# Optimization experiments

Measured on AMD Instinct MI355X. Metric: run time of the kernel, lower is better.

The kernel has to match this reference:

```python
import jax, jax.numpy as jnp
import numpy as np


def setup_inputs() -> dict:
    key = jax.random.key(0)
    ks = jax.random.split(key, 8)
    B, IN, H, OUT = 8192, 1024, 2048, 1024
    SIGMA_MIN, SIGMA_MAX, PHASE = 0.9, 0.999, 2.0 * np.pi
    # recurrence decay params, initialized as in the torch module
    rng = np.random.RandomState(0)
    u1 = rng.random_sample(H)
    u2 = rng.random_sample(H)
    v = -0.5 * np.log(u1 * (SIGMA_MAX ** 2 - SIGMA_MIN ** 2) + SIGMA_MIN ** 2)
    theta = u2 * PHASE
    scale_b = 1.0 / np.sqrt(IN)
    scale_c = 1.0 / np.sqrt(H)
    return {
        "x": jax.random.normal(ks[0], (B, IN), dtype=jnp.float32),
        "h_prev": jax.random.normal(ks[1], (B, H), dtype=jnp.float32),
        "Br": jax.random.normal(ks[2], (H, IN), dtype=jnp.float32) * scale_b,
        "Bi": jax.random.normal(ks[3], (H, IN), dtype=jnp.float32) * scale_b,
        "Cr": jax.random.normal(ks[4], (OUT, H), dtype=jnp.float32) * scale_c,
        "Ci": jax.random.normal(ks[5], (OUT, H), dtype=jnp.float32) * scale_c,
        "v_log": jnp.asarray(np.log(v), dtype=jnp.float32),
        "theta_log": jnp.asarray(np.log(theta), dtype=jnp.float32),
    }


def reference(x, h_prev, Br, Bi, Cr, Ci, v_log, theta_log):
    # effective diagonal recurrence weight w = exp(-exp(v_log) + i*exp(theta_log))
    mag = jnp.exp(-jnp.exp(v_log))            # [H]
    ang = jnp.exp(theta_log)                  # [H]
    wr = mag * jnp.cos(ang)
    wi = mag * jnp.sin(ang)
    # h = B(x) + h_prev * w  (h_prev is real -> imag part comes only from wi)
    # complexLinear on real x: real = x@Br^T, imag = x@Bi^T
    hr = jnp.einsum('bi,hi->bh', x, Br) + h_prev * wr   # [B,H]
    hi = jnp.einsum('bi,hi->bh', x, Bi) + h_prev * wi   # [B,H]
    # out = Re(C(h)) = hr@Cr^T - hi@Ci^T
    out = jnp.einsum('bh,oh->bo', hr, Cr) - jnp.einsum('bh,oh->bo', hi, Ci)
    return out
```

## Files before the change

kernel.cpp:

```cpp
#include <hip/hip_runtime.h>
#include <stdint.h>

typedef unsigned short u16;
typedef short bf16x8 __attribute__((ext_vector_type(8)));
typedef float f32x4 __attribute__((ext_vector_type(4)));

typedef void as1_void __attribute__((address_space(1)));
typedef void as3_void __attribute__((address_space(3)));

__device__ inline u16 f32_to_bf16(float f) {
    uint32_t u = __builtin_bit_cast(uint32_t, f);
    u += 0x7fffu + ((u >> 16) & 1u);
    return (u16)(u >> 16);
}

__device__ inline void gld_lds16(const void* g, void* l) {
    __builtin_amdgcn_global_load_lds((as1_void*)g, (as3_void*)l, 16, 0, 0);
}



__global__ void prep_kernel(const float* __restrict__ Cr, const float* __restrict__ Ci,
                            const float* __restrict__ Br, const float* __restrict__ Bi,
                            const float* __restrict__ v_log, const float* __restrict__ th_log,
                            u16* __restrict__ Ccat, u16* __restrict__ Bcat,
                            u16* __restrict__ Cwbf)
{
    __shared__ float t[32][33];
    const int b = blockIdx.x, tid = threadIdx.x;

    if (b < 4096) {
        int i = b * 256 + tid;
        int e = i * 4;
        int o = e >> 12;
        int k = e & 4095;
        float4 f; float s;
        if (k < 2048) { f = *(const float4*)(Cr + (size_t)o * 2048 + k);          s =  1.f; }
        else          { f = *(const float4*)(Ci + (size_t)o * 2048 + (k - 2048)); s = -1.f; }
        ushort4 u;
        u.x = f32_to_bf16(s * f.x); u.y = f32_to_bf16(s * f.y);
        u.z = f32_to_bf16(s * f.z); u.w = f32_to_bf16(s * f.w);
        ((ushort4*)Ccat)[i] = u;
    } else if (b < 8192) {
        int b2 = b - 4096;
        const float* src = (b2 & 2048) ? Bi : Br;
        int colOff = (b2 & 2048) ? 2048 : 0;
        int c0 = (b2 & 31) * 32, r0 = ((b2 >> 5) & 63) * 32;
        int tx = tid & 31, ty = tid >> 5;
#pragma unroll
        for (int j = 0; j < 4; j++)
            t[ty + j * 8][tx] = src[(size_t)(r0 + ty + j * 8) * 1024 + c0 + tx];
        __syncthreads();
#pragma unroll
        for (int j = 0; j < 4; j++)
            Bcat[(size_t)(c0 + ty + j * 8) * 4096 + colOff + r0 + tx] =
                f32_to_bf16(t[tx][ty + j * 8]);
    } else {
        int j = (b - 8192) * 256 + tid;
        int e = j * 4;
        int o = e >> 11;
        int h = e & 2047;
        float4 cr = *(const float4*)(Cr + (size_t)o * 2048 + h);
        float4 ci = *(const float4*)(Ci + (size_t)o * 2048 + h);
        float4 vl = *(const float4*)(v_log + h);
        float4 tl = *(const float4*)(th_log + h);
        float mag, ang, wr, wi;
        ushort4 u;
        mag = expf(-expf(vl.x)); ang = expf(tl.x); wr = mag * cosf(ang); wi = mag * sinf(ang);
        u.x = f32_to_bf16(cr.x * wr - ci.x * wi);
        mag = expf(-expf(vl.y)); ang = expf(tl.y); wr = mag * cosf(ang); wi = mag * sinf(ang);
        u.y = f32_to_bf16(cr.y * wr - ci.y * wi);
        mag = expf(-expf(vl.z)); ang = expf(tl.z); wr = mag * cosf(ang); wi = mag * sinf(ang);
        u.z = f32_to_bf16(cr.z * wr - ci.z * wi);
        mag = expf(-expf(vl.w)); ang = expf(tl.w); wr = mag * cosf(ang); wi = mag * sinf(ang);
        u.w = f32_to_bf16(cr.w * wr - ci.w * wi);
        ((ushort4*)Cwbf)[j] = u;
    }
}


__global__ void reduce_cast_kernel(const float* __restrict__ partials,
                                   const float* __restrict__ x,
                                   const float* __restrict__ h_prev,
                                   u16* __restrict__ Wmain,
                                   u16* __restrict__ x_bf,
                                   u16* __restrict__ hp_bf)
{
    const int b = blockIdx.x, tid = threadIdx.x;
    if (b < 1024) {
        int i = b * 256 + tid;
        int e = i * 4;
        float4 s = *(const float4*)(partials + e);
#pragma unroll
        for (int z = 1; z < 8; z++) {
            float4 p = *(const float4*)(partials + ((size_t)z << 20) + e);
            s.x += p.x; s.y += p.y; s.z += p.z; s.w += p.w;
        }
        ushort4 u;
        u.x = f32_to_bf16(s.x); u.y = f32_to_bf16(s.y);
        u.z = f32_to_bf16(s.z); u.w = f32_to_bf16(s.w);
        ((ushort4*)Wmain)[i] = u;
    } else if (b < 9216) {
        int i = (b - 1024) * 256 + tid;
        float4 f = ((const float4*)x)[i];
        ushort4 o;
        o.x = f32_to_bf16(f.x); o.y = f32_to_bf16(f.y);
        o.z = f32_to_bf16(f.z); o.w = f32_to_bf16(f.w);
        ((ushort4*)x_bf)[i] = o;
    } else {
        int i = (b - 9216) * 256 + tid;
        float4 f = ((const float4*)h_prev)[i];
        ushort4 o;
        o.x = f32_to_bf16(f.x); o.y = f32_to_bf16(f.y);
        o.z = f32_to_bf16(f.z); o.w = f32_to_bf16(f.w);
        ((ushort4*)hp_bf)[i] = o;
    }
}


__global__ void reduce_only_kernel(const float* __restrict__ partials,
                                   u16* __restrict__ Wmain) {
    int i = blockIdx.x * blockDim.x + threadIdx.x;
    int e = i * 4;
    float4 s = *(const float4*)(partials + e);
#pragma unroll
    for (int z = 1; z < 8; z++) {
        float4 p = *(const float4*)(partials + ((size_t)z << 20) + e);
        s.x += p.x; s.y += p.y; s.z += p.z; s.w += p.w;
    }
    ushort4 u;
    u.x = f32_to_bf16(s.x); u.y = f32_to_bf16(s.y);
    u.z = f32_to_bf16(s.z); u.w = f32_to_bf16(s.w);
    ((ushort4*)Wmain)[i] = u;
}

__global__ void cast_both_kernel(const float* __restrict__ x,
                                 const float* __restrict__ h_prev,
                                 u16* __restrict__ dst) {
    const int n4x = 8192 * 1024 / 4;
    int i = blockIdx.x * blockDim.x + threadIdx.x;
    float4 f = (i < n4x) ? ((const float4*)x)[i] : ((const float4*)h_prev)[i - n4x];
    ushort4 o;
    o.x = f32_to_bf16(f.x); o.y = f32_to_bf16(f.y);
    o.z = f32_to_bf16(f.z); o.w = f32_to_bf16(f.w);
    ((ushort4*)dst)[i] = o;
}


__global__ __launch_bounds__(256)
void gemm_splitk_kernel(const u16* __restrict__ A, const u16* __restrict__ B,
                        float* __restrict__ partials)
{
    __shared__ __align__(16) u16 ldsA[128 * 64];
    __shared__ __align__(16) u16 ldsB[128 * 64];
    const int K = 4096;

    const int tid = threadIdx.x, wid = tid >> 6, lane = tid & 63;
    const int quad = lane >> 4, l16 = lane & 15;
    const int wm = wid >> 1, wn = wid & 1;
    const int bm = blockIdx.y, bn = blockIdx.x, bz = blockIdx.z;
    const int kb = bz * 512;

    const u16* gA[4]; const u16* gB[4];
    u16 *lA[4], *lB[4];
#pragma unroll
    for (int t = 0; t < 4; t++) {
        int s = wid * 256 + t * 64 + lane;
        int sr = s >> 3;
        int sj = (s & 7) ^ (sr & 7);
        lA[t] = ldsA + s * 8;
        lB[t] = ldsB + s * 8;
        gA[t] = A + (size_t)(bm * 128 + sr) * K + sj * 8 + kb;
        gB[t] = B + (size_t)(bn * 128 + sr) * K + sj * 8 + kb;
    }

    const f32x4 fz = {0.f, 0.f, 0.f, 0.f};
    f32x4 acc[4][4];
#pragma unroll
    for (int i = 0; i < 4; i++)
#pragma unroll
        for (int j = 0; j < 4; j++) acc[i][j] = fz;

    for (int k0 = 0; k0 < 512; k0 += 64) {
        __syncthreads();
#pragma unroll
        for (int t = 0; t < 4; t++) {
            gld_lds16(gA[t] + k0, lA[t]);
            gld_lds16(gB[t] + k0, lB[t]);
        }
        __syncthreads();
#pragma unroll
        for (int ks = 0; ks < 2; ks++) {
            bf16x8 af[4], bfr[4];
#pragma unroll
            for (int i = 0; i < 4; i++) {
                int r = wm * 64 + i * 16 + l16;
                af[i] = *(const bf16x8*)(ldsA + (r * 8 + ((ks * 4 + quad) ^ (r & 7))) * 8);
            }
#pragma unroll
            for (int j = 0; j < 4; j++) {
                int r = wn * 64 + j * 16 + l16;
                bfr[j] = *(const bf16x8*)(ldsB + (r * 8 + ((ks * 4 + quad) ^ (r & 7))) * 8);
            }
#pragma unroll
            for (int i = 0; i < 4; i++)
#pragma unroll
                for (int j = 0; j < 4; j++)
                    acc[i][j] = __builtin_amdgcn_mfma_f32_16x16x32_bf16(af[i], bfr[j], acc[i][j], 0, 0, 0);
        }
    }

    float* P = partials + ((size_t)bz << 20);
    const int gm = bm * 128 + wm * 64, gn = bn * 128 + wn * 64;
#pragma unroll
    for (int i = 0; i < 4; i++)
#pragma unroll
        for (int j = 0; j < 4; j++) {
            int col = gn + j * 16 + l16;
#pragma unroll
            for (int r = 0; r < 4; r++)
                P[(size_t)(gm + i * 16 + quad * 4 + r) * 1024 + col] = acc[i][j][r];
        }
}


__global__ __launch_bounds__(512)
void gemm_main_kernel(const u16* __restrict__ Axb, const u16* __restrict__ Ahb,
                      const u16* __restrict__ Bw,  const u16* __restrict__ Bcw,
                      float* __restrict__ out)
{
    __shared__ __align__(16) u16 lds[3][24576];

    const int tid = threadIdx.x, wid = tid >> 6, lane = tid & 63;
    const int quad = lane >> 4, l16 = lane & 15;
    const int wm = wid >> 1, wn = wid & 1;
    const int id = blockIdx.x;
    const int bm = id & 31, bn = id >> 5;

    int srA[4], sjA[4], srB[2], sjB[2];
#pragma unroll
    for (int q = 0; q < 4; q++) {
        int s = q * 512 + tid;
        srA[q] = s >> 3;
        sjA[q] = (s & 7) ^ (srA[q] & 7);
    }
#pragma unroll
    for (int q = 0; q < 2; q++) {
        int s = q * 512 + tid;
        srB[q] = s >> 3;
        sjB[q] = (s & 7) ^ (srB[q] & 7);
    }

    u16* buf0 = &lds[0][0];
    u16* buf1 = &lds[1][0];
    u16* buf2 = &lds[2][0];

    const f32x4 fz = {0.f, 0.f, 0.f, 0.f};
    f32x4 acc[4][4];
#pragma unroll
    for (int i = 0; i < 4; i++)
#pragma unroll
        for (int j = 0; j < 4; j++) acc[i][j] = fz;

    auto stage = [&](int tt, u16* buf) {
        const u16* Ab; const u16* Bb; int KS, koff;
        if (tt < 16) { Ab = Axb; Bb = Bw;  KS = 1024; koff = tt * 64; }
        else         { Ab = Ahb; Bb = Bcw; KS = 2048; koff = (tt - 16) * 64; }
#pragma unroll
        for (int q = 0; q < 4; q++)
            gld_lds16(Ab + (size_t)(bm * 256 + srA[q]) * KS + koff + sjA[q] * 8,
                      buf + (q * 512 + tid) * 8);
#pragma unroll
        for (int q = 0; q < 2; q++)
            gld_lds16(Bb + (size_t)(bn * 128 + srB[q]) * KS + koff + sjB[q] * 8,
                      buf + 16384 + (q * 512 + tid) * 8);
    };

    auto compute = [&](const u16* buf) {
#pragma unroll
        for (int ks = 0; ks < 2; ks++) {
            bf16x8 af[4], bfr[4];
#pragma unroll
            for (int i = 0; i < 4; i++) {
                int r = wm * 64 + i * 16 + l16;
                af[i] = *(const bf16x8*)(buf + (r * 8 + ((ks * 4 + quad) ^ (r & 7))) * 8);
            }
#pragma unroll
            for (int j = 0; j < 4; j++) {
                int r = wn * 64 + j * 16 + l16;
                bfr[j] = *(const bf16x8*)(buf + 16384 + (r * 8 + ((ks * 4 + quad) ^ (r & 7))) * 8);
            }
            __builtin_amdgcn_s_setprio(1);
#pragma unroll
            for (int i = 0; i < 4; i++)
#pragma unroll
                for (int j = 0; j < 4; j++)
                    acc[i][j] = __builtin_amdgcn_mfma_f32_16x16x32_bf16(af[i], bfr[j], acc[i][j], 0, 0, 0);
            __builtin_amdgcn_s_setprio(0);
        }
    };

#define PUBLISH(N)                                          \
    asm volatile("s_waitcnt vmcnt(" #N ")" ::: "memory");   \
    __builtin_amdgcn_s_barrier();                           \
    asm volatile("" ::: "memory")

    stage(0, buf0);
    stage(1, buf1);
    PUBLISH(6);

#pragma unroll 1
    for (int it = 0; it < 15; it++) {
        stage(3 * it + 2, buf2); compute(buf0); PUBLISH(6);
        stage(3 * it + 3, buf0); compute(buf1); PUBLISH(6);
        stage(3 * it + 4, buf1); compute(buf2); PUBLISH(6);
    }
    stage(47, buf2); compute(buf0); PUBLISH(6);
    compute(buf1); PUBLISH(0);
    compute(buf2);
#undef PUBLISH

    const int gm = bm * 256 + wm * 64, gn = bn * 128 + wn * 64;
#pragma unroll
    for (int i = 0; i < 4; i++)
#pragma unroll
        for (int j = 0; j < 4; j++) {
            int col = gn + j * 16 + l16;
#pragma unroll
            for (int r = 0; r < 4; r++)
                out[(size_t)(gm + i * 16 + quad * 4 + r) * 1024 + col] = acc[i][j][r];
        }
}


extern "C" void kernel_launch(void* const* d_in, const int* in_sizes, int n_in,
                              void* d_out, int out_size, void* d_ws, size_t ws_size,
                              hipStream_t stream)
{
    const float* x      = (const float*)d_in[0];
    const float* h_prev = (const float*)d_in[1];
    const float* Br     = (const float*)d_in[2];
    const float* Bi     = (const float*)d_in[3];
    const float* Cr     = (const float*)d_in[4];
    const float* Ci     = (const float*)d_in[5];
    const float* v_log  = (const float*)d_in[6];
    const float* th_log = (const float*)d_in[7];
    float* out = (float*)d_out;

    const size_t MB = 1024 * 1024;
    if (ws_size < 54 * MB) return;
    const bool big = (ws_size >= 86 * MB);

    char* ws = (char*)d_ws;
    u16*   Ccat     = (u16*)ws;
    u16*   Bcat     = (u16*)(ws + 8 * MB);
    float* partials = (float*)(ws + 16 * MB);
    u16*   x_bf     = (u16*)ws;
    u16*   Wmain    = (u16*)(ws + 48 * MB);
    u16*   Cwbf     = (u16*)(ws + 50 * MB);
    u16*   hp_bf    = big ? (u16*)(ws + 54 * MB) : (u16*)(ws + 16 * MB);

    prep_kernel<<<10240, 256, 0, stream>>>(Cr, Ci, Br, Bi, v_log, th_log,
                                           Ccat, Bcat, Cwbf);
    gemm_splitk_kernel<<<dim3(8, 8, 8), 256, 0, stream>>>(Ccat, Bcat, partials);
    if (big) {
        reduce_cast_kernel<<<25600, 256, 0, stream>>>(partials, x, h_prev,
                                                      Wmain, x_bf, hp_bf);
    } else {
        reduce_only_kernel<<<1024, 256, 0, stream>>>(partials, Wmain);
        cast_both_kernel<<<24576, 256, 0, stream>>>(x, h_prev, x_bf);
    }
    gemm_main_kernel<<<256, 512, 0, stream>>>(x_bf, hp_bf, Wmain, Cwbf, out);
}
```

Baseline: 246.2 us.

## Fuse fp32-to-bf16 activation cast into main GEMM A-tile loading

Removes the separate cast kernel for x and h_prev. The main GEMM now loads the fp32 activations into registers, converts them to bf16 and writes them into LDS itself, while B tiles still use direct global-to-LDS loads. This avoids writing and rereading roughly 48 MB of bf16 intermediates and drops a kernel launch. In exchange the GEMM reads twice the bytes for A, adds VALU conversion work and register pressure, and replaces the vmcnt-based pipelining with full __syncthreads, which may expose load latency.

```diff
diff --git a/kernel.cpp b/kernel.cpp
--- a/kernel.cpp
+++ b/kernel.cpp
@@ -79,45 +79,6 @@
 }
 
 
-__global__ void reduce_cast_kernel(const float* __restrict__ partials,
-                                   const float* __restrict__ x,
-                                   const float* __restrict__ h_prev,
-                                   u16* __restrict__ Wmain,
-                                   u16* __restrict__ x_bf,
-                                   u16* __restrict__ hp_bf)
-{
-    const int b = blockIdx.x, tid = threadIdx.x;
-    if (b < 1024) {
-        int i = b * 256 + tid;
-        int e = i * 4;
-        float4 s = *(const float4*)(partials + e);
-#pragma unroll
-        for (int z = 1; z < 8; z++) {
-            float4 p = *(const float4*)(partials + ((size_t)z << 20) + e);
-            s.x += p.x; s.y += p.y; s.z += p.z; s.w += p.w;
-        }
-        ushort4 u;
-        u.x = f32_to_bf16(s.x); u.y = f32_to_bf16(s.y);
-        u.z = f32_to_bf16(s.z); u.w = f32_to_bf16(s.w);
-        ((ushort4*)Wmain)[i] = u;
-    } else if (b < 9216) {
-        int i = (b - 1024) * 256 + tid;
-        float4 f = ((const float4*)x)[i];
-        ushort4 o;
-        o.x = f32_to_bf16(f.x); o.y = f32_to_bf16(f.y);
-        o.z = f32_to_bf16(f.z); o.w = f32_to_bf16(f.w);
-        ((ushort4*)x_bf)[i] = o;
-    } else {
-        int i = (b - 9216) * 256 + tid;
-        float4 f = ((const float4*)h_prev)[i];
-        ushort4 o;
-        o.x = f32_to_bf16(f.x); o.y = f32_to_bf16(f.y);
-        o.z = f32_to_bf16(f.z); o.w = f32_to_bf16(f.w);
-        ((ushort4*)hp_bf)[i] = o;
-    }
-}
-
-
 __global__ void reduce_only_kernel(const float* __restrict__ partials,
                                    u16* __restrict__ Wmain) {
     int i = blockIdx.x * blockDim.x + threadIdx.x;
@@ -132,18 +93,6 @@
     u.x = f32_to_bf16(s.x); u.y = f32_to_bf16(s.y);
     u.z = f32_to_bf16(s.z); u.w = f32_to_bf16(s.w);
     ((ushort4*)Wmain)[i] = u;
-}
-
-__global__ void cast_both_kernel(const float* __restrict__ x,
-                                 const float* __restrict__ h_prev,
-                                 u16* __restrict__ dst) {
-    const int n4x = 8192 * 1024 / 4;
-    int i = blockIdx.x * blockDim.x + threadIdx.x;
-    float4 f = (i < n4x) ? ((const float4*)x)[i] : ((const float4*)h_prev)[i - n4x];
-    ushort4 o;
-    o.x = f32_to_bf16(f.x); o.y = f32_to_bf16(f.y);
-    o.z = f32_to_bf16(f.z); o.w = f32_to_bf16(f.w);
-    ((ushort4*)dst)[i] = o;
 }
 
 
@@ -225,7 +174,7 @@
 
 
 __global__ __launch_bounds__(512)
-void gemm_main_kernel(const u16* __restrict__ Axb, const u16* __restrict__ Ahb,
+void gemm_main_kernel(const float* __restrict__ Xf, const float* __restrict__ Hf,
                       const u16* __restrict__ Bw,  const u16* __restrict__ Bcw,
                       float* __restrict__ out)
 {
@@ -262,18 +211,43 @@
 #pragma unroll
         for (int j = 0; j < 4; j++) acc[i][j] = fz;
 
-    auto stage = [&](int tt, u16* buf) {
-        const u16* Ab; const u16* Bb; int KS, koff;
-        if (tt < 16) { Ab = Axb; Bb = Bw;  KS = 1024; koff = tt * 64; }
-        else         { Ab = Ahb; Bb = Bcw; KS = 2048; koff = (tt - 16) * 64; }
-#pragma unroll
-        for (int q = 0; q < 4; q++)
-            gld_lds16(Ab + (size_t)(bm * 256 + srA[q]) * KS + koff + sjA[q] * 8,
-                      buf + (q * 512 + tid) * 8);
+    auto stageB = [&](int tt, u16* buf) {
+        const u16* Bb; int KS, koff;
+        if (tt < 16) { Bb = Bw;  KS = 1024; koff = tt * 64; }
+        else         { Bb = Bcw; KS = 2048; koff = (tt - 16) * 64; }
 #pragma unroll
         for (int q = 0; q < 2; q++)
             gld_lds16(Bb + (size_t)(bn * 128 + srB[q]) * KS + koff + sjB[q] * 8,
                       buf + 16384 + (q * 512 + tid) * 8);
+    };
+
+    float4 areg[4][2];
+    auto loadA = [&](int tt) {
+        const float* Af; int KS, koff;
+        if (tt < 16) { Af = Xf; KS = 1024; koff = tt * 64; }
+        else         { Af = Hf; KS = 2048; koff = (tt - 16) * 64; }
+#pragma unroll
+        for (int q = 0; q < 4; q++) {
+            const float* p = Af + (size_t)(bm * 256 + srA[q]) * KS + koff + sjA[q] * 8;
+            areg[q][0] = *(const float4*)(p);
+            areg[q][1] = *(const float4*)(p + 4);
+        }
+    };
+
+    auto writeA = [&](u16* buf) {
+#pragma unroll
+        for (int q = 0; q < 4; q++) {
+            bf16x8 v;
+            v[0] = (short)f32_to_bf16(areg[q][0].x);
+            v[1] = (short)f32_to_bf16(areg[q][0].y);
+            v[2] = (short)f32_to_bf16(areg[q][0].z);
+            v[3] = (short)f32_to_bf16(areg[q][0].w);
+            v[4] = (short)f32_to_bf16(areg[q][1].x);
+            v[5] = (short)f32_to_bf16(areg[q][1].y);
+            v[6] = (short)f32_to_bf16(areg[q][1].z);
+            v[7] = (short)f32_to_bf16(areg[q][1].w);
+            *(bf16x8*)(buf + ((size_t)q * 512 + tid) * 8) = v;
+        }
     };
 
     auto compute = [&](const u16* buf) {
@@ -300,25 +274,19 @@
         }
     };
 
-#define PUBLISH(N)                                          \
-    asm volatile("s_waitcnt vmcnt(" #N ")" ::: "memory");   \
-    __builtin_amdgcn_s_barrier();                           \
-    asm volatile("" ::: "memory")
-
-    stage(0, buf0);
-    stage(1, buf1);
-    PUBLISH(6);
+    stageB(0, buf0); loadA(0); writeA(buf0);
+    stageB(1, buf1); loadA(1); writeA(buf1);
+    __syncthreads();
 
 #pragma unroll 1
     for (int it = 0; it < 15; it++) {
-        stage(3 * it + 2, buf2); compute(buf0); PUBLISH(6);
-        stage(3 * it + 3, buf0); compute(buf1); PUBLISH(6);
-        stage(3 * it + 4, buf1); compute(buf2); PUBLISH(6);
-    }
-    stage(47, buf2); compute(buf0); PUBLISH(6);
-    compute(buf1); PUBLISH(0);
+        stageB(3 * it + 2, buf2); loadA(3 * it + 2); compute(buf0); writeA(buf2); __syncthreads();
+        stageB(3 * it + 3, buf0); loadA(3 * it + 3); compute(buf1); writeA(buf0); __syncthreads();
+        stageB(3 * it + 4, buf1); loadA(3 * it + 4); compute(buf2); writeA(buf1); __syncthreads();
+    }
+    stageB(47, buf2); loadA(47); compute(buf0); writeA(buf2); __syncthreads();
+    compute(buf1);
     compute(buf2);
-#undef PUBLISH
 
     const int gm = bm * 256 + wm * 64, gn = bn * 128 + wn * 64;
 #pragma unroll
@@ -349,26 +317,17 @@
 
     const size_t MB = 1024 * 1024;
     if (ws_size < 54 * MB) return;
-    const bool big = (ws_size >= 86 * MB);
 
     char* ws = (char*)d_ws;
     u16*   Ccat     = (u16*)ws;
     u16*   Bcat     = (u16*)(ws + 8 * MB);
     float* partials = (float*)(ws + 16 * MB);
-    u16*   x_bf     = (u16*)ws;
     u16*   Wmain    = (u16*)(ws + 48 * MB);
     u16*   Cwbf     = (u16*)(ws + 50 * MB);
-    u16*   hp_bf    = big ? (u16*)(ws + 54 * MB) : (u16*)(ws + 16 * MB);
 
     prep_kernel<<<10240, 256, 0, stream>>>(Cr, Ci, Br, Bi, v_log, th_log,
                                            Ccat, Bcat, Cwbf);
     gemm_splitk_kernel<<<dim3(8, 8, 8), 256, 0, stream>>>(Ccat, Bcat, partials);
-    if (big) {
-        reduce_cast_kernel<<<25600, 256, 0, stream>>>(partials, x, h_prev,
-                                                      Wmain, x_bf, hp_bf);
-    } else {
-        reduce_only_kernel<<<1024, 256, 0, stream>>>(partials, Wmain);
-        cast_both_kernel<<<24576, 256, 0, stream>>>(x, h_prev, x_bf);
-    }
-    gemm_main_kernel<<<256, 512, 0, stream>>>(x_bf, hp_bf, Wmain, Cwbf, out);
-}
+    reduce_only_kernel<<<1024, 256, 0, stream>>>(partials, Wmain);
+    gemm_main_kernel<<<256, 512, 0, stream>>>(x, h_prev, Wmain, Cwbf, out);
+}
```

Result: slower. 291.0 us (+18.2%).

## Fuse split-K weight GEMM with activation bf16 cast in one launch

Applied to the files above, without the earlier changes.

Adds a combined kernel where the first 512 blocks compute the split-K weight-product GEMM and the remaining blocks cast x and h_prev to bf16 with a grid-stride loop. The memory-bound cast is meant to overlap with the compute-bound GEMM instead of running in a separate serialized phase, and the reduce kernel becomes reduce-only. It needs a larger workspace (102 MB) to keep separate buffers for x_bf and hp_bf, and otherwise falls back to the old path. Cast blocks may contend for bandwidth and compute units with the GEMM blocks.

```diff
diff --git a/kernel.cpp b/kernel.cpp
--- a/kernel.cpp
+++ b/kernel.cpp
@@ -79,6 +79,120 @@
 }
 
 
+__device__ __forceinline__
+void splitk_block(const u16* __restrict__ A, const u16* __restrict__ B,
+                  float* __restrict__ partials,
+                  int bm, int bn, int bz, int tid,
+                  u16* ldsA, u16* ldsB)
+{
+    const int K = 4096;
+    const int wid = tid >> 6, lane = tid & 63;
+    const int quad = lane >> 4, l16 = lane & 15;
+    const int wm = wid >> 1, wn = wid & 1;
+    const int kb = bz * 512;
+
+    const u16* gA[4]; const u16* gB[4];
+    u16 *lA[4], *lB[4];
+#pragma unroll
+    for (int t = 0; t < 4; t++) {
+        int s = wid * 256 + t * 64 + lane;
+        int sr = s >> 3;
+        int sj = (s & 7) ^ (sr & 7);
+        lA[t] = ldsA + s * 8;
+        lB[t] = ldsB + s * 8;
+        gA[t] = A + (size_t)(bm * 128 + sr) * K + sj * 8 + kb;
+        gB[t] = B + (size_t)(bn * 128 + sr) * K + sj * 8 + kb;
+    }
+
+    const f32x4 fz = {0.f, 0.f, 0.f, 0.f};
+    f32x4 acc[4][4];
+#pragma unroll
+    for (int i = 0; i < 4; i++)
+#pragma unroll
+        for (int j = 0; j < 4; j++) acc[i][j] = fz;
+
+    for (int k0 = 0; k0 < 512; k0 += 64) {
+        __syncthreads();
+#pragma unroll
+        for (int t = 0; t < 4; t++) {
+            gld_lds16(gA[t] + k0, lA[t]);
+            gld_lds16(gB[t] + k0, lB[t]);
+        }
+        __syncthreads();
+#pragma unroll
+        for (int ks = 0; ks < 2; ks++) {
+            bf16x8 af[4], bfr[4];
+#pragma unroll
+            for (int i = 0; i < 4; i++) {
+                int r = wm * 64 + i * 16 + l16;
+                af[i] = *(const bf16x8*)(ldsA + (r * 8 + ((ks * 4 + quad) ^ (r & 7))) * 8);
+            }
+#pragma unroll
+            for (int j = 0; j < 4; j++) {
+                int r = wn * 64 + j * 16 + l16;
+                bfr[j] = *(const bf16x8*)(ldsB + (r * 8 + ((ks * 4 + quad) ^ (r & 7))) * 8);
+            }
+#pragma unroll
+            for (int i = 0; i < 4; i++)
+#pragma unroll
+                for (int j = 0; j < 4; j++)
+                    acc[i][j] = __builtin_amdgcn_mfma_f32_16x16x32_bf16(af[i], bfr[j], acc[i][j], 0, 0, 0);
+        }
+    }
+
+    float* P = partials + ((size_t)bz << 20);
+    const int gm = bm * 128 + wm * 64, gn = bn * 128 + wn * 64;
+#pragma unroll
+    for (int i = 0; i < 4; i++)
+#pragma unroll
+        for (int j = 0; j < 4; j++) {
+            int col = gn + j * 16 + l16;
+#pragma unroll
+            for (int r = 0; r < 4; r++)
+                P[(size_t)(gm + i * 16 + quad * 4 + r) * 1024 + col] = acc[i][j][r];
+        }
+}
+
+__global__ __launch_bounds__(256)
+void gemm_splitk_kernel(const u16* __restrict__ A, const u16* __restrict__ B,
+                        float* __restrict__ partials)
+{
+    __shared__ __align__(16) u16 ldsA[128 * 64];
+    __shared__ __align__(16) u16 ldsB[128 * 64];
+    splitk_block(A, B, partials, blockIdx.y, blockIdx.x, blockIdx.z, threadIdx.x,
+                 ldsA, ldsB);
+}
+
+__global__ __launch_bounds__(256)
+void splitk_cast_kernel(const u16* __restrict__ A, const u16* __restrict__ B,
+                        float* __restrict__ partials,
+                        const float* __restrict__ x, const float* __restrict__ h_prev,
+                        u16* __restrict__ x_bf, u16* __restrict__ hp_bf)
+{
+    __shared__ __align__(16) u16 ldsA[128 * 64];
+    __shared__ __align__(16) u16 ldsB[128 * 64];
+    const int id = blockIdx.x, tid = threadIdx.x;
+    if (id < 512) {
+        splitk_block(A, B, partials, (id >> 3) & 7, id & 7, id >> 6, tid,
+                     ldsA, ldsB);
+        return;
+    }
+    const int cid = id - 512;
+    const int n4x = 8192 * 1024 / 4;
+    const int n4  = n4x + 8192 * 2048 / 4;
+#pragma unroll 1
+    for (int j = cid * 256 + tid; j < n4; j += 2048 * 256) {
+        float4 f; ushort4 o;
+        if (j < n4x) { f = ((const float4*)x)[j]; }
+        else         { f = ((const float4*)h_prev)[j - n4x]; }
+        o.x = f32_to_bf16(f.x); o.y = f32_to_bf16(f.y);
+        o.z = f32_to_bf16(f.z); o.w = f32_to_bf16(f.w);
+        if (j < n4x) ((ushort4*)x_bf)[j] = o;
+        else         ((ushort4*)hp_bf)[j - n4x] = o;
+    }
+}
+
+
 __global__ void reduce_cast_kernel(const float* __restrict__ partials,
                                    const float* __restrict__ x,
                                    const float* __restrict__ h_prev,
@@ -117,7 +231,6 @@
     }
 }
 
-
 __global__ void reduce_only_kernel(const float* __restrict__ partials,
                                    u16* __restrict__ Wmain) {
     int i = blockIdx.x * blockDim.x + threadIdx.x;
@@ -147,83 +260,6 @@
 }
 
 
-__global__ __launch_bounds__(256)
-void gemm_splitk_kernel(const u16* __restrict__ A, const u16* __restrict__ B,
-                        float* __restrict__ partials)
-{
-    __shared__ __align__(16) u16 ldsA[128 * 64];
-    __shared__ __align__(16) u16 ldsB[128 * 64];
-    const int K = 4096;
-
-    const int tid = threadIdx.x, wid = tid >> 6, lane = tid & 63;
-    const int quad = lane >> 4, l16 = lane & 15;
-    const int wm = wid >> 1, wn = wid & 1;
-    const int bm = blockIdx.y, bn = blockIdx.x, bz = blockIdx.z;
-    const int kb = bz * 512;
-
-    const u16* gA[4]; const u16* gB[4];
-    u16 *lA[4], *lB[4];
-#pragma unroll
-    for (int t = 0; t < 4; t++) {
-        int s = wid * 256 + t * 64 + lane;
-        int sr = s >> 3;
-        int sj = (s & 7) ^ (sr & 7);
-        lA[t] = ldsA + s * 8;
-        lB[t] = ldsB + s * 8;
-        gA[t] = A + (size_t)(bm * 128 + sr) * K + sj * 8 + kb;
-        gB[t] = B + (size_t)(bn * 128 + sr) * K + sj * 8 + kb;
-    }
-
-    const f32x4 fz = {0.f, 0.f, 0.f, 0.f};
-    f32x4 acc[4][4];
-#pragma unroll
-    for (int i = 0; i < 4; i++)
-#pragma unroll
-        for (int j = 0; j < 4; j++) acc[i][j] = fz;
-
-    for (int k0 = 0; k0 < 512; k0 += 64) {
-        __syncthreads();
-#pragma unroll
-        for (int t = 0; t < 4; t++) {
-            gld_lds16(gA[t] + k0, lA[t]);
-            gld_lds16(gB[t] + k0, lB[t]);
-        }
-        __syncthreads();
-#pragma unroll
-        for (int ks = 0; ks < 2; ks++) {
-            bf16x8 af[4], bfr[4];
-#pragma unroll
-            for (int i = 0; i < 4; i++) {
-                int r = wm * 64 + i * 16 + l16;
-                af[i] = *(const bf16x8*)(ldsA + (r * 8 + ((ks * 4 + quad) ^ (r & 7))) * 8);
-            }
-#pragma unroll
-            for (int j = 0; j < 4; j++) {
-                int r = wn * 64 + j * 16 + l16;
-                bfr[j] = *(const bf16x8*)(ldsB + (r * 8 + ((ks * 4 + quad) ^ (r & 7))) * 8);
-            }
-#pragma unroll
-            for (int i = 0; i < 4; i++)
-#pragma unroll
-                for (int j = 0; j < 4; j++)
-                    acc[i][j] = __builtin_amdgcn_mfma_f32_16x16x32_bf16(af[i], bfr[j], acc[i][j], 0, 0, 0);
-        }
-    }
-
-    float* P = partials + ((size_t)bz << 20);
-    const int gm = bm * 128 + wm * 64, gn = bn * 128 + wn * 64;
-#pragma unroll
-    for (int i = 0; i < 4; i++)
-#pragma unroll
-        for (int j = 0; j < 4; j++) {
-            int col = gn + j * 16 + l16;
-#pragma unroll
-            for (int r = 0; r < 4; r++)
-                P[(size_t)(gm + i * 16 + quad * 4 + r) * 1024 + col] = acc[i][j][r];
-        }
-}
-
-
 __global__ __launch_bounds__(512)
 void gemm_main_kernel(const u16* __restrict__ Axb, const u16* __restrict__ Ahb,
                       const u16* __restrict__ Bw,  const u16* __restrict__ Bcw,
@@ -349,26 +385,35 @@
 
     const size_t MB = 1024 * 1024;
     if (ws_size < 54 * MB) return;
-    const bool big = (ws_size >= 86 * MB);
+    const bool big2 = (ws_size >= 102 * MB);
+    const bool big  = (ws_size >= 86 * MB);
 
     char* ws = (char*)d_ws;
     u16*   Ccat     = (u16*)ws;
     u16*   Bcat     = (u16*)(ws + 8 * MB);
     float* partials = (float*)(ws + 16 * MB);
-    u16*   x_bf     = (u16*)ws;
     u16*   Wmain    = (u16*)(ws + 48 * MB);
     u16*   Cwbf     = (u16*)(ws + 50 * MB);
-    u16*   hp_bf    = big ? (u16*)(ws + 54 * MB) : (u16*)(ws + 16 * MB);
+    u16*   x_bf     = big2 ? (u16*)(ws + 54 * MB) : (u16*)ws;
+    u16*   hp_bf    = big2 ? (u16*)(ws + 70 * MB)
+                    : big  ? (u16*)(ws + 54 * MB)
+                           : (u16*)(ws + 16 * MB);
 
     prep_kernel<<<10240, 256, 0, stream>>>(Cr, Ci, Br, Bi, v_log, th_log,
                                            Ccat, Bcat, Cwbf);
-    gemm_splitk_kernel<<<dim3(8, 8, 8), 256, 0, stream>>>(Ccat, Bcat, partials);
-    if (big) {
-        reduce_cast_kernel<<<25600, 256, 0, stream>>>(partials, x, h_prev,
-                                                      Wmain, x_bf, hp_bf);
+    if (big2) {
+        splitk_cast_kernel<<<2560, 256, 0, stream>>>(Ccat, Bcat, partials,
+                                                     x, h_prev, x_bf, hp_bf);
+        reduce_only_kernel<<<1024, 256, 0, stream>>>(partials, Wmain);
     } else {
-        reduce_only_kernel<<<1024, 256, 0, stream>>>(partials, Wmain);
-        cast_both_kernel<<<24576, 256, 0, stream>>>(x, h_prev, x_bf);
+        gemm_splitk_kernel<<<dim3(8, 8, 8), 256, 0, stream>>>(Ccat, Bcat, partials);
+        if (big) {
+            reduce_cast_kernel<<<25600, 256, 0, stream>>>(partials, x, h_prev,
+                                                          Wmain, x_bf, hp_bf);
+        } else {
+            reduce_only_kernel<<<1024, 256, 0, stream>>>(partials, Wmain);
+            cast_both_kernel<<<24576, 256, 0, stream>>>(x, h_prev, x_bf);
+        }
     }
     gemm_main_kernel<<<256, 512, 0, stream>>>(x_bf, hp_bf, Wmain, Cwbf, out);
 }
```

Result: slower. 254.4 us (+3.3%).
